# Kernel optimization log

Hardware: AMD Instinct MI355X
Metric: run time of the kernel (lower is better)

Reference implementation:

```python
import jax, jax.numpy as jnp
import numpy as np

N_NODES = 50000
N_EDGES = 1000000
IN_DIM, HID_DIM, OUT_DIM = 128, 64, 16


def setup_inputs() -> dict:
    key = jax.random.key(0)
    k1, k2, k3, k4 = jax.random.split(key, 4)
    x = jax.random.normal(k1, (N_NODES, IN_DIM), dtype=jnp.float32)
    edge_index = jax.random.randint(k2, (2, N_EDGES), 0, N_NODES, dtype=jnp.int64)
    # Glorot-style scaling for weights, zero bias (PyG GCNConv default init style)
    W1 = jax.random.normal(k3, (IN_DIM, HID_DIM), dtype=jnp.float32) * (1.0 / np.sqrt(IN_DIM))
    b1 = jnp.zeros((HID_DIM,), dtype=jnp.float32)
    W2 = jax.random.normal(k4, (HID_DIM, OUT_DIM), dtype=jnp.float32) * (1.0 / np.sqrt(HID_DIM))
    b2 = jnp.zeros((OUT_DIM,), dtype=jnp.float32)
    return {"x": x, "edge_index": edge_index, "W1": W1, "b1": b1, "W2": W2, "b2": b2}


def gcn_conv(x, src, dst, W, b, num_nodes):
    """PyG GCNConv: add self loops, symmetric deg^{-1/2} normalization,
    linear transform, gather-scale-scatter aggregation, bias."""
    # degree includes self loops (src/dst already augmented by caller)
    deg = jax.ops.segment_sum(jnp.ones_like(dst, dtype=x.dtype), dst, num_segments=num_nodes)
    dinv = jnp.where(deg > 0, deg ** -0.5, 0.0)
    norm = dinv[src] * dinv[dst]            # [E']
    h = x @ W                                # [N, F_out] transform before aggregation
    msg = h[src] * norm[:, None]             # gather + scale
    out = jax.ops.segment_sum(msg, dst, num_segments=num_nodes)  # scatter-add
    return out + b


def reference(x, edge_index, W1, b1, W2, b2):
    n = x.shape[0]
    loops = jnp.arange(n, dtype=edge_index.dtype)
    src = jnp.concatenate([edge_index[0], loops])
    dst = jnp.concatenate([edge_index[1], loops])
    h = gcn_conv(x, src, dst, W1, b1, n)
    h = jax.nn.relu(h)
    out = gcn_conv(h, src, dst, W2, b2, n)
    return out
```

## Files before the change

kernel.cpp:

```cpp
#include <hip/hip_runtime.h>
#include <hip/hip_bf16.h>

#define IN_DIM 128
#define HID_DIM 64
#define OUT_DIM 16

#define SSHIFT 7
#define SMASK 127
#define CHUNK 16384
#define CBLK 1024

static __device__ __forceinline__ unsigned short f2bf(float f) {
    unsigned u = __float_as_uint(f);
    unsigned r = u + 0x7fffu + ((u >> 16) & 1u);
    return (unsigned short)(r >> 16);
}
static __device__ __forceinline__ unsigned packbf2(float a, float b) {
    return (unsigned)f2bf(a) | ((unsigned)f2bf(b) << 16);
}
static __device__ __forceinline__ float bflo(unsigned v) { return __uint_as_float(v << 16); }
static __device__ __forceinline__ float bfhi(unsigned v) { return __uint_as_float(v & 0xffff0000u); }

__global__ __launch_bounds__(CBLK) void passA(const int* __restrict__ dst,
                                              int* __restrict__ cm,
                                              int E, int NS, int NSP) {
    __shared__ int cnt[512];
    int t = threadIdx.x;
    for (int s = t; s < NS; s += CBLK) cnt[s] = 0;
    __syncthreads();
    int base = blockIdx.x * CHUNK;
    #pragma unroll 4
    for (int k = 0; k < CHUNK; k += CBLK) {
        int i = base + k + t;
        if (i < E) atomicAdd(&cnt[dst[i] >> SSHIFT], 1);
    }
    __syncthreads();
    for (int s = t; s < NS; s += CBLK) cm[blockIdx.x * NSP + s] = cnt[s];
}

__global__ __launch_bounds__(64) void passB1(int* __restrict__ cm, int* __restrict__ tot,
                                             int B, int NSP) {
    __shared__ int sv[64];
    int t = threadIdx.x, s = blockIdx.x;
    int v = (t < B) ? cm[t * NSP + s] : 0;
    sv[t] = v;
    __syncthreads();
    for (int off = 1; off < 64; off <<= 1) {
        int tmp = (t >= off) ? sv[t - off] : 0;
        __syncthreads();
        sv[t] += tmp;
        __syncthreads();
    }
    if (t < B) cm[t * NSP + s] = sv[t] - v;
    if (t == 63) tot[s] = sv[63];
}

__global__ __launch_bounds__(512) void passB2(const int* __restrict__ tot,
                                              int* __restrict__ sbase, int NS) {
    __shared__ int sv[512];
    int t = threadIdx.x;
    int v = (t < NS) ? tot[t] : 0;
    sv[t] = v;
    __syncthreads();
    for (int off = 1; off < 512; off <<= 1) {
        int tmp = (t >= off) ? sv[t - off] : 0;
        __syncthreads();
        sv[t] += tmp;
        __syncthreads();
    }
    if (t < NS) sbase[t] = sv[t] - v;
}

__global__ __launch_bounds__(CBLK) void passC(const int* __restrict__ src,
                                              const int* __restrict__ dst,
                                              const int* __restrict__ cm,
                                              const int* __restrict__ sbase,
                                              int* __restrict__ eb,
                                              int E, int NS, int NSP) {
    __shared__ int cur[512];
    int t = threadIdx.x, b = blockIdx.x;
    for (int s = t; s < NS; s += CBLK) cur[s] = sbase[s] + cm[b * NSP + s];
    __syncthreads();
    int base = b * CHUNK;
    #pragma unroll 4
    for (int k = 0; k < CHUNK; k += CBLK) {
        int i = base + k + t;
        if (i < E) {
            int d = dst[i];
            int s = d >> SSHIFT;
            int pos = atomicAdd(&cur[s], 1);
            eb[pos] = src[i] | ((d & SMASK) << 17);
        }
    }
}

__global__ __launch_bounds__(256) void passD(const int* __restrict__ eb,
                                             const int* __restrict__ sbase,
                                             const int* __restrict__ tot,
                                             int* __restrict__ csr_src,
                                             int* __restrict__ row_ptr,
                                             float* __restrict__ dinv,
                                             int N, int E, int NS) {
    __shared__ int deg[128], incl[128], cur[128];
    int s = blockIdx.x, t = threadIdx.x;
    if (t < 128) deg[t] = 0;
    __syncthreads();
    int b0 = sbase[s], cnt = tot[s];
    for (int k = t; k < cnt; k += 256) atomicAdd(&deg[eb[b0 + k] >> 17], 1);
    __syncthreads();
    if (t < 128) incl[t] = deg[t];
    __syncthreads();
    for (int off = 1; off < 128; off <<= 1) {
        int tmp = 0;
        if (t < 128 && t >= off) tmp = incl[t - off];
        __syncthreads();
        if (t < 128) incl[t] += tmp;
        __syncthreads();
    }
    if (t < 128) {
        int loff = incl[t] - deg[t];
        cur[t] = b0 + loff;
        int n = (s << SSHIFT) + t;
        if (n < N) {
            row_ptr[n] = b0 + loff;
            dinv[n] = rsqrtf((float)(deg[t] + 1));
        }
    }
    if (s == NS - 1 && t == 0) row_ptr[N] = E;
    __syncthreads();
    for (int k = t; k < cnt; k += 256) {
        int v = eb[b0 + k];
        int dl = v >> 17;
        int p = atomicAdd(&cur[dl], 1);
        csr_src[p] = v & 0x1FFFF;
    }
}

__global__ __launch_bounds__(256) void gemm1_kernel(const float* __restrict__ x,
                                                    const float* __restrict__ W1,
                                                    const float* __restrict__ dinv,
                                                    unsigned* __restrict__ h1u, int N) {
    __shared__ __align__(16) float sW[IN_DIM * HID_DIM];
    __shared__ __align__(16) float sx[16 * IN_DIM];
    int t = threadIdx.x;
    int node0 = blockIdx.x * 16;

    const float4* W4  = (const float4*)W1;
    float4*       sW4 = (float4*)sW;
    for (int i = t; i < (IN_DIM * HID_DIM) / 4; i += 256) sW4[i] = W4[i];

    const float4* x4  = (const float4*)x;
    float4*       sx4 = (float4*)sx;
    for (int i = t; i < (16 * IN_DIM) / 4; i += 256) {
        int r = i >> 5, c = i & 31;
        int n = node0 + r; if (n >= N) n = 0;
        sx4[(r << 5) + c] = x4[(size_t)n * 32 + c];
    }
    __syncthreads();

    int ln = t >> 4, jj = t & 15;
    int n = node0 + ln;
    float4 acc = {0.f, 0.f, 0.f, 0.f};
    const float* xr = sx + ln * IN_DIM;
    #pragma unroll 4
    for (int k = 0; k < IN_DIM; ++k) {
        float  xk = xr[k];
        float4 wv = ((const float4*)(sW + k * HID_DIM))[jj];
        acc.x += xk * wv.x; acc.y += xk * wv.y; acc.z += xk * wv.z; acc.w += xk * wv.w;
    }
    if (n <= N) {
        float dn = (n < N) ? dinv[n] : 0.f;
        uint2 pv;
        pv.x = packbf2(acc.x * dn, acc.y * dn);
        pv.y = packbf2(acc.z * dn, acc.w * dn);
        ((uint2*)(h1u + (size_t)n * 32))[jj] = pv;
    }
}

__global__ __launch_bounds__(256) void agg1_kernel(const unsigned* __restrict__ h1u,
                                                   const int* __restrict__ row_ptr,
                                                   const int* __restrict__ csr_src,
                                                   const float* __restrict__ dinv,
                                                   const float* __restrict__ b1,
                                                   unsigned* __restrict__ h1au, int N) {
    int t = threadIdx.x;
    int n = blockIdx.x * 4 + (t >> 6);
    if (n >= N) return;
    int lane = t & 63;
    int es = lane >> 3;
    int dg = lane & 7;

    int e0 = row_ptr[n], e1 = row_ptr[n + 1];
    const uint4* rb = (const uint4*)h1u;

    float a0 = 0.f, a1 = 0.f, a2 = 0.f, a3 = 0.f,
          a4 = 0.f, a5 = 0.f, a6 = 0.f, a7 = 0.f;

    for (int base = e0 - 1; base < e1; base += 64) {
        int idx = base + lane;
        int sld = N;
        if (idx == e0 - 1) sld = n;
        else if (idx < e1) sld = csr_src[idx];
        int lim = e1 - base;
        int nr = (lim + 7) >> 3;
        nr = (nr + 1) & ~1;
        for (int r = 0; r < nr; r += 2) {
            int sA = __shfl(sld, (r << 3) + es);
            int sB = __shfl(sld, ((r + 1) << 3) + es);
            uint4 vA = rb[(size_t)sA * 8 + dg];
            uint4 vB = rb[(size_t)sB * 8 + dg];
            a0 += bflo(vA.x) + bflo(vB.x);
            a1 += bfhi(vA.x) + bfhi(vB.x);
            a2 += bflo(vA.y) + bflo(vB.y);
            a3 += bfhi(vA.y) + bfhi(vB.y);
            a4 += bflo(vA.z) + bflo(vB.z);
            a5 += bfhi(vA.z) + bfhi(vB.z);
            a6 += bflo(vA.w) + bflo(vB.w);
            a7 += bfhi(vA.w) + bfhi(vB.w);
        }
    }
    #pragma unroll
    for (int m = 8; m <= 32; m <<= 1) {
        a0 += __shfl_xor(a0, m); a1 += __shfl_xor(a1, m);
        a2 += __shfl_xor(a2, m); a3 += __shfl_xor(a3, m);
        a4 += __shfl_xor(a4, m); a5 += __shfl_xor(a5, m);
        a6 += __shfl_xor(a6, m); a7 += __shfl_xor(a7, m);
    }
    if (es == 0) {
        float dn = dinv[n];
        float4 bA = ((const float4*)b1)[2 * dg];
        float4 bB = ((const float4*)b1)[2 * dg + 1];
        float r0 = fmaxf(fmaf(dn, a0, bA.x), 0.f);
        float r1 = fmaxf(fmaf(dn, a1, bA.y), 0.f);
        float r2 = fmaxf(fmaf(dn, a2, bA.z), 0.f);
        float r3 = fmaxf(fmaf(dn, a3, bA.w), 0.f);
        float r4 = fmaxf(fmaf(dn, a4, bB.x), 0.f);
        float r5 = fmaxf(fmaf(dn, a5, bB.y), 0.f);
        float r6 = fmaxf(fmaf(dn, a6, bB.z), 0.f);
        float r7 = fmaxf(fmaf(dn, a7, bB.w), 0.f);
        uint4 pv;
        pv.x = packbf2(r0, r1); pv.y = packbf2(r2, r3);
        pv.z = packbf2(r4, r5); pv.w = packbf2(r6, r7);
        ((uint4*)h1au)[(size_t)n * 8 + dg] = pv;
    }
}

__global__ __launch_bounds__(256) void gemm2_kernel(const unsigned* __restrict__ h1au,
                                                    const float* __restrict__ W2,
                                                    const float* __restrict__ dinv,
                                                    unsigned* __restrict__ h2u, int N) {
    __shared__ __align__(16) float sW[HID_DIM * OUT_DIM];
    __shared__ __align__(16) float sx[16 * HID_DIM];
    int t = threadIdx.x;
    int node0 = blockIdx.x * 16;

    ((float4*)sW)[t] = ((const float4*)W2)[t];
    for (int i = t; i < 512; i += 256) {
        int r = i >> 5, c = i & 31;
        int n = node0 + r; if (n >= N) n = 0;
        unsigned v = h1au[(size_t)n * 32 + c];
        float2 f; f.x = bflo(v); f.y = bfhi(v);
        *(float2*)(sx + r * HID_DIM + 2 * c) = f;
    }
    __syncthreads();

    int ln = t >> 4, j = t & 15;
    float acc = 0.f;
    const float* xr = sx + ln * HID_DIM;
    #pragma unroll 8
    for (int k = 0; k < HID_DIM; ++k) acc += xr[k] * sW[k * OUT_DIM + j];
    int n = node0 + ln;
    float other = __shfl_xor(acc, 1);
    if (n <= N && (j & 1) == 0) {
        float dn = (n < N) ? dinv[n] : 0.f;
        h2u[(size_t)n * 8 + (j >> 1)] = packbf2(acc * dn, other * dn);
    }
}

__global__ __launch_bounds__(256) void agg2_kernel(const unsigned* __restrict__ h2u,
                                                   const int* __restrict__ row_ptr,
                                                   const int* __restrict__ csr_src,
                                                   const float* __restrict__ dinv,
                                                   const float* __restrict__ b2,
                                                   float* __restrict__ out, int N) {
    int t = threadIdx.x;
    int n = blockIdx.x * 4 + (t >> 6);
    if (n >= N) return;
    int lane = t & 63;
    int es = lane >> 2;
    int dg = lane & 3;

    int e0 = row_ptr[n], e1 = row_ptr[n + 1];
    const uint2* rb = (const uint2*)h2u;

    float a0 = 0.f, a1 = 0.f, a2 = 0.f, a3 = 0.f;

    for (int base = e0 - 1; base < e1; base += 64) {
        int idx = base + lane;
        int sld = N;
        if (idx == e0 - 1) sld = n;
        else if (idx < e1) sld = csr_src[idx];
        int lim = e1 - base;
        int nr = (lim + 15) >> 4;
        nr = (nr + 1) & ~1;
        for (int r = 0; r < nr; r += 2) {
            int sA = __shfl(sld, (r << 4) + es);
            int sB = __shfl(sld, ((r + 1) << 4) + es);
            uint2 vA = rb[(size_t)sA * 4 + dg];
            uint2 vB = rb[(size_t)sB * 4 + dg];
            a0 += bflo(vA.x) + bflo(vB.x);
            a1 += bfhi(vA.x) + bfhi(vB.x);
            a2 += bflo(vA.y) + bflo(vB.y);
            a3 += bfhi(vA.y) + bfhi(vB.y);
        }
    }
    #pragma unroll
    for (int m = 4; m <= 32; m <<= 1) {
        a0 += __shfl_xor(a0, m); a1 += __shfl_xor(a1, m);
        a2 += __shfl_xor(a2, m); a3 += __shfl_xor(a3, m);
    }
    if (es == 0) {
        float dn = dinv[n];
        float4 bb = ((const float4*)b2)[dg];
        float4 r;
        r.x = fmaf(dn, a0, bb.x);
        r.y = fmaf(dn, a1, bb.y);
        r.z = fmaf(dn, a2, bb.z);
        r.w = fmaf(dn, a3, bb.w);
        ((float4*)out)[(size_t)n * 4 + dg] = r;
    }
}

extern "C" void kernel_launch(void* const* d_in, const int* in_sizes, int n_in,
                              void* d_out, int out_size, void* d_ws, size_t ws_size,
                              hipStream_t stream) {
    const float* x  = (const float*)d_in[0];
    const int*   ei = (const int*)d_in[1];
    const float* W1 = (const float*)d_in[2];
    const float* b1 = (const float*)d_in[3];
    const float* W2 = (const float*)d_in[4];
    const float* b2 = (const float*)d_in[5];
    float* out = (float*)d_out;

    const int N = in_sizes[0] / IN_DIM;
    const int E = in_sizes[1] / 2;
    const int* src = ei;
    const int* dst = ei + E;

    const int NS  = (N + SMASK) >> SSHIFT;
    const int NSP = NS + 1;
    const int BC  = (E + CHUNK - 1) / CHUNK;

    char* w = (char*)d_ws;
    auto alloc = [&](size_t bytes) -> void* {
        void* p = (void*)w;
        w += (bytes + 255) & ~(size_t)255;
        return p;
    };
    int*      cm      = (int*)     alloc((size_t)BC * NSP * 4);
    int*      tot     = (int*)     alloc((size_t)NS * 4);
    int*      sbase   = (int*)     alloc((size_t)NS * 4);
    int*      eb      = (int*)     alloc((size_t)E * 4);
    int*      csr_src = (int*)     alloc((size_t)E * 4);
    int*      row_ptr = (int*)     alloc((size_t)(N + 1) * 4);
    float*    dinv    = (float*)   alloc((size_t)N * 4);
    unsigned* h1u     = (unsigned*)alloc((size_t)(N + 1) * 32 * 4);
    unsigned* h1au    = (unsigned*)alloc((size_t)(N + 1) * 32 * 4);
    unsigned* h2u     = (unsigned*)alloc((size_t)(N + 1) * 8 * 4);

    const int GB = (N + 16) / 16;
    const int AB = (N + 3) / 4;

    passA <<<BC, CBLK, 0, stream>>>(dst, cm, E, NS, NSP);
    passB1<<<NS, 64,   0, stream>>>(cm, tot, BC, NSP);
    passB2<<<1,  512,  0, stream>>>(tot, sbase, NS);
    passC <<<BC, CBLK, 0, stream>>>(src, dst, cm, sbase, eb, E, NS, NSP);
    passD <<<NS, 256,  0, stream>>>(eb, sbase, tot, csr_src, row_ptr, dinv, N, E, NS);

    gemm1_kernel<<<GB, 256, 0, stream>>>(x, W1, dinv, h1u, N);
    agg1_kernel<<<AB, 256, 0, stream>>>(h1u, row_ptr, csr_src, dinv, b1, h1au, N);
    gemm2_kernel<<<GB, 256, 0, stream>>>(h1au, W2, dinv, h2u, N);
    agg2_kernel<<<AB, 256, 0, stream>>>(h2u, row_ptr, csr_src, dinv, b2, out, N);
}
```

Baseline: 187.4 us.

## Fuse second-layer GEMM into layer-1 aggregation and shrink counting-sort chunks

Folds the 64x16 W2 transform into agg1_kernel. After the shuffle reduction every lane holds the full 64-wide aggregated row, so each lane applies ReLU and bias, multiplies its 8 features by a slice of W2 held in shared memory, and reduces over 8 lanes to write h2 directly. This removes the h1au intermediate buffer, its write and reread, and one kernel launch. Separately, the counting-sort pass uses smaller chunks and blocks (4096/256 instead of 16384/1024), giving more blocks, with the per-bucket scan widened to 256. The padding row of h2 is zeroed inside passB2 because gemm2, which used to write it, is gone.

```diff
diff --git a/kernel.cpp b/kernel.cpp
--- a/kernel.cpp
+++ b/kernel.cpp
@@ -7,8 +7,8 @@
 
 #define SSHIFT 7
 #define SMASK 127
-#define CHUNK 16384
-#define CBLK 1024
+#define CHUNK 4096
+#define CBLK 256
 
 static __device__ __forceinline__ unsigned short f2bf(float f) {
     unsigned u = __float_as_uint(f);
@@ -38,25 +38,27 @@
     for (int s = t; s < NS; s += CBLK) cm[blockIdx.x * NSP + s] = cnt[s];
 }
 
-__global__ __launch_bounds__(64) void passB1(int* __restrict__ cm, int* __restrict__ tot,
-                                             int B, int NSP) {
-    __shared__ int sv[64];
+__global__ __launch_bounds__(256) void passB1(int* __restrict__ cm, int* __restrict__ tot,
+                                              int B, int NSP) {
+    __shared__ int sv[256];
     int t = threadIdx.x, s = blockIdx.x;
     int v = (t < B) ? cm[t * NSP + s] : 0;
     sv[t] = v;
     __syncthreads();
-    for (int off = 1; off < 64; off <<= 1) {
+    for (int off = 1; off < 256; off <<= 1) {
         int tmp = (t >= off) ? sv[t - off] : 0;
         __syncthreads();
         sv[t] += tmp;
         __syncthreads();
     }
     if (t < B) cm[t * NSP + s] = sv[t] - v;
-    if (t == 63) tot[s] = sv[63];
+    if (t == 255) tot[s] = sv[255];
 }
 
 __global__ __launch_bounds__(512) void passB2(const int* __restrict__ tot,
-                                              int* __restrict__ sbase, int NS) {
+                                              int* __restrict__ sbase,
+                                              unsigned* __restrict__ h2u_dummy,
+                                              int NS) {
     __shared__ int sv[512];
     int t = threadIdx.x;
     int v = (t < NS) ? tot[t] : 0;
@@ -69,6 +71,7 @@
         __syncthreads();
     }
     if (t < NS) sbase[t] = sv[t] - v;
+    if (t >= 504) h2u_dummy[t - 504] = 0u;
 }
 
 __global__ __launch_bounds__(CBLK) void passC(const int* __restrict__ src,
@@ -182,8 +185,13 @@
                                                    const int* __restrict__ csr_src,
                                                    const float* __restrict__ dinv,
                                                    const float* __restrict__ b1,
-                                                   unsigned* __restrict__ h1au, int N) {
-    int t = threadIdx.x;
+                                                   const float* __restrict__ W2,
+                                                   unsigned* __restrict__ h2u, int N) {
+    __shared__ __align__(16) float sW[HID_DIM * OUT_DIM];
+    int t = threadIdx.x;
+    ((float4*)sW)[t] = ((const float4*)W2)[t];
+    __syncthreads();
+
     int n = blockIdx.x * 4 + (t >> 6);
     if (n >= N) return;
     int lane = t & 63;
@@ -226,54 +234,35 @@
         a4 += __shfl_xor(a4, m); a5 += __shfl_xor(a5, m);
         a6 += __shfl_xor(a6, m); a7 += __shfl_xor(a7, m);
     }
-    if (es == 0) {
-        float dn = dinv[n];
-        float4 bA = ((const float4*)b1)[2 * dg];
-        float4 bB = ((const float4*)b1)[2 * dg + 1];
-        float r0 = fmaxf(fmaf(dn, a0, bA.x), 0.f);
-        float r1 = fmaxf(fmaf(dn, a1, bA.y), 0.f);
-        float r2 = fmaxf(fmaf(dn, a2, bA.z), 0.f);
-        float r3 = fmaxf(fmaf(dn, a3, bA.w), 0.f);
-        float r4 = fmaxf(fmaf(dn, a4, bB.x), 0.f);
-        float r5 = fmaxf(fmaf(dn, a5, bB.y), 0.f);
-        float r6 = fmaxf(fmaf(dn, a6, bB.z), 0.f);
-        float r7 = fmaxf(fmaf(dn, a7, bB.w), 0.f);
-        uint4 pv;
-        pv.x = packbf2(r0, r1); pv.y = packbf2(r2, r3);
-        pv.z = packbf2(r4, r5); pv.w = packbf2(r6, r7);
-        ((uint4*)h1au)[(size_t)n * 8 + dg] = pv;
-    }
-}
-
-__global__ __launch_bounds__(256) void gemm2_kernel(const unsigned* __restrict__ h1au,
-                                                    const float* __restrict__ W2,
-                                                    const float* __restrict__ dinv,
-                                                    unsigned* __restrict__ h2u, int N) {
-    __shared__ __align__(16) float sW[HID_DIM * OUT_DIM];
-    __shared__ __align__(16) float sx[16 * HID_DIM];
-    int t = threadIdx.x;
-    int node0 = blockIdx.x * 16;
-
-    ((float4*)sW)[t] = ((const float4*)W2)[t];
-    for (int i = t; i < 512; i += 256) {
-        int r = i >> 5, c = i & 31;
-        int n = node0 + r; if (n >= N) n = 0;
-        unsigned v = h1au[(size_t)n * 32 + c];
-        float2 f; f.x = bflo(v); f.y = bfhi(v);
-        *(float2*)(sx + r * HID_DIM + 2 * c) = f;
-    }
-    __syncthreads();
-
-    int ln = t >> 4, j = t & 15;
-    float acc = 0.f;
-    const float* xr = sx + ln * HID_DIM;
-    #pragma unroll 8
-    for (int k = 0; k < HID_DIM; ++k) acc += xr[k] * sW[k * OUT_DIM + j];
-    int n = node0 + ln;
-    float other = __shfl_xor(acc, 1);
-    if (n <= N && (j & 1) == 0) {
-        float dn = (n < N) ? dinv[n] : 0.f;
-        h2u[(size_t)n * 8 + (j >> 1)] = packbf2(acc * dn, other * dn);
+    float dn = dinv[n];
+    float4 bA = ((const float4*)b1)[2 * dg];
+    float4 bB = ((const float4*)b1)[2 * dg + 1];
+    float r0 = fmaxf(fmaf(dn, a0, bA.x), 0.f);
+    float r1 = fmaxf(fmaf(dn, a1, bA.y), 0.f);
+    float r2 = fmaxf(fmaf(dn, a2, bA.z), 0.f);
+    float r3 = fmaxf(fmaf(dn, a3, bA.w), 0.f);
+    float r4 = fmaxf(fmaf(dn, a4, bB.x), 0.f);
+    float r5 = fmaxf(fmaf(dn, a5, bB.y), 0.f);
+    float r6 = fmaxf(fmaf(dn, a6, bB.z), 0.f);
+    float r7 = fmaxf(fmaf(dn, a7, bB.w), 0.f);
+
+    const float* wrow = sW + (8 * dg) * OUT_DIM + 2 * es;
+    float p0 = 0.f, p1 = 0.f;
+    #pragma unroll
+    for (int i = 0; i < 8; ++i) {
+        float2 wv = *(const float2*)(wrow + i * OUT_DIM);
+        float ri = (i == 0) ? r0 : (i == 1) ? r1 : (i == 2) ? r2 : (i == 3) ? r3
+                 : (i == 4) ? r4 : (i == 5) ? r5 : (i == 6) ? r6 : r7;
+        p0 = fmaf(ri, wv.x, p0);
+        p1 = fmaf(ri, wv.y, p1);
+    }
+    #pragma unroll
+    for (int m = 1; m <= 4; m <<= 1) {
+        p0 += __shfl_xor(p0, m);
+        p1 += __shfl_xor(p1, m);
+    }
+    if (dg == 0) {
+        h2u[(size_t)n * 8 + es] = packbf2(p0 * dn, p1 * dn);
     }
 }
 
@@ -357,7 +346,7 @@
         w += (bytes + 255) & ~(size_t)255;
         return p;
     };
-    int*      cm      = (int*)     alloc((size_t)BC * NSP * 4);
+    int*      cm      = (int*)     alloc((size_t)256 * NSP * 4);
     int*      tot     = (int*)     alloc((size_t)NS * 4);
     int*      sbase   = (int*)     alloc((size_t)NS * 4);
     int*      eb      = (int*)     alloc((size_t)E * 4);
@@ -365,20 +354,18 @@
     int*      row_ptr = (int*)     alloc((size_t)(N + 1) * 4);
     float*    dinv    = (float*)   alloc((size_t)N * 4);
     unsigned* h1u     = (unsigned*)alloc((size_t)(N + 1) * 32 * 4);
-    unsigned* h1au    = (unsigned*)alloc((size_t)(N + 1) * 32 * 4);
     unsigned* h2u     = (unsigned*)alloc((size_t)(N + 1) * 8 * 4);
 
     const int GB = (N + 16) / 16;
     const int AB = (N + 3) / 4;
 
     passA <<<BC, CBLK, 0, stream>>>(dst, cm, E, NS, NSP);
-    passB1<<<NS, 64,   0, stream>>>(cm, tot, BC, NSP);
-    passB2<<<1,  512,  0, stream>>>(tot, sbase, NS);
+    passB1<<<NS, 256,  0, stream>>>(cm, tot, BC, NSP);
+    passB2<<<1,  512,  0, stream>>>(tot, sbase, h2u + (size_t)N * 8, NS);
     passC <<<BC, CBLK, 0, stream>>>(src, dst, cm, sbase, eb, E, NS, NSP);
     passD <<<NS, 256,  0, stream>>>(eb, sbase, tot, csr_src, row_ptr, dinv, N, E, NS);
 
     gemm1_kernel<<<GB, 256, 0, stream>>>(x, W1, dinv, h1u, N);
-    agg1_kernel<<<AB, 256, 0, stream>>>(h1u, row_ptr, csr_src, dinv, b1, h1au, N);
-    gemm2_kernel<<<GB, 256, 0, stream>>>(h1au, W2, dinv, h2u, N);
+    agg1_kernel<<<AB, 256, 0, stream>>>(h1u, row_ptr, csr_src, dinv, b1, W2, h2u, N);
     agg2_kernel<<<AB, 256, 0, stream>>>(h2u, row_ptr, csr_src, dinv, b2, out, N);
 }
```

Measured after the change: 195.0 us. +4.0%, slower.

## Drop the global bucket-scan kernel and shrink histogram chunks for more blocks

Applied to the files above, without the earlier changes.

Removes the single-block passB2 scan launch. Each passC block now recomputes the bucket prefix over per-bucket totals in shared memory, and passD computes its own base offset by reducing the totals of the preceding buckets. Histogram chunks shrink from 16384 to 4096 edges with 256-thread blocks, so passA and passC get more blocks (about 245 instead of 62), and passB1 now scans up to 256 block counts. This trades one serialized kernel launch for redundant per-block scan work. It relies on the block count staying at or below 256, since cm is sized for 256 rows.

```diff
diff --git a/kernel.cpp b/kernel.cpp
--- a/kernel.cpp
+++ b/kernel.cpp
@@ -7,8 +7,8 @@
 
 #define SSHIFT 7
 #define SMASK 127
-#define CHUNK 16384
-#define CBLK 1024
+#define CHUNK 4096
+#define CBLK 256
 
 static __device__ __forceinline__ unsigned short f2bf(float f) {
     unsigned u = __float_as_uint(f);
@@ -38,48 +38,46 @@
     for (int s = t; s < NS; s += CBLK) cm[blockIdx.x * NSP + s] = cnt[s];
 }
 
-__global__ __launch_bounds__(64) void passB1(int* __restrict__ cm, int* __restrict__ tot,
-                                             int B, int NSP) {
-    __shared__ int sv[64];
+__global__ __launch_bounds__(256) void passB1(int* __restrict__ cm, int* __restrict__ tot,
+                                              int B, int NSP) {
+    __shared__ int sv[256];
     int t = threadIdx.x, s = blockIdx.x;
     int v = (t < B) ? cm[t * NSP + s] : 0;
     sv[t] = v;
     __syncthreads();
-    for (int off = 1; off < 64; off <<= 1) {
+    for (int off = 1; off < 256; off <<= 1) {
         int tmp = (t >= off) ? sv[t - off] : 0;
         __syncthreads();
         sv[t] += tmp;
         __syncthreads();
     }
     if (t < B) cm[t * NSP + s] = sv[t] - v;
-    if (t == 63) tot[s] = sv[63];
-}
-
-__global__ __launch_bounds__(512) void passB2(const int* __restrict__ tot,
-                                              int* __restrict__ sbase, int NS) {
-    __shared__ int sv[512];
-    int t = threadIdx.x;
-    int v = (t < NS) ? tot[t] : 0;
-    sv[t] = v;
-    __syncthreads();
-    for (int off = 1; off < 512; off <<= 1) {
-        int tmp = (t >= off) ? sv[t - off] : 0;
-        __syncthreads();
-        sv[t] += tmp;
-        __syncthreads();
-    }
-    if (t < NS) sbase[t] = sv[t] - v;
+    if (t == 255) tot[s] = sv[255];
 }
 
 __global__ __launch_bounds__(CBLK) void passC(const int* __restrict__ src,
                                               const int* __restrict__ dst,
                                               const int* __restrict__ cm,
-                                              const int* __restrict__ sbase,
+                                              const int* __restrict__ tot,
                                               int* __restrict__ eb,
                                               int E, int NS, int NSP) {
+    __shared__ int sb[512];
     __shared__ int cur[512];
     int t = threadIdx.x, b = blockIdx.x;
-    for (int s = t; s < NS; s += CBLK) cur[s] = sbase[s] + cm[b * NSP + s];
+    int i0 = t, i1 = t + 256;
+    int v0 = (i0 < NS) ? tot[i0] : 0;
+    int v1 = (i1 < NS) ? tot[i1] : 0;
+    sb[i0] = v0; sb[i1] = v1;
+    __syncthreads();
+    for (int off = 1; off < 512; off <<= 1) {
+        int t0 = (i0 >= off) ? sb[i0 - off] : 0;
+        int t1 = (i1 >= off) ? sb[i1 - off] : 0;
+        __syncthreads();
+        sb[i0] += t0; sb[i1] += t1;
+        __syncthreads();
+    }
+    if (i0 < NS) cur[i0] = (sb[i0] - v0) + cm[b * NSP + i0];
+    if (i1 < NS) cur[i1] = (sb[i1] - v1) + cm[b * NSP + i1];
     __syncthreads();
     int base = b * CHUNK;
     #pragma unroll 4
@@ -95,17 +93,25 @@
 }
 
 __global__ __launch_bounds__(256) void passD(const int* __restrict__ eb,
-                                             const int* __restrict__ sbase,
                                              const int* __restrict__ tot,
                                              int* __restrict__ csr_src,
                                              int* __restrict__ row_ptr,
                                              float* __restrict__ dinv,
                                              int N, int E, int NS) {
+    __shared__ int red[256];
     __shared__ int deg[128], incl[128], cur[128];
     int s = blockIdx.x, t = threadIdx.x;
     if (t < 128) deg[t] = 0;
-    __syncthreads();
-    int b0 = sbase[s], cnt = tot[s];
+    int part = 0;
+    for (int k = t; k < s; k += 256) part += tot[k];
+    red[t] = part;
+    __syncthreads();
+    for (int off = 128; off >= 1; off >>= 1) {
+        if (t < off) red[t] += red[t + off];
+        __syncthreads();
+    }
+    int b0 = red[0];
+    int cnt = tot[s];
     for (int k = t; k < cnt; k += 256) atomicAdd(&deg[eb[b0 + k] >> 17], 1);
     __syncthreads();
     if (t < 128) incl[t] = deg[t];
@@ -357,9 +363,8 @@
         w += (bytes + 255) & ~(size_t)255;
         return p;
     };
-    int*      cm      = (int*)     alloc((size_t)BC * NSP * 4);
+    int*      cm      = (int*)     alloc((size_t)256 * NSP * 4);
     int*      tot     = (int*)     alloc((size_t)NS * 4);
-    int*      sbase   = (int*)     alloc((size_t)NS * 4);
     int*      eb      = (int*)     alloc((size_t)E * 4);
     int*      csr_src = (int*)     alloc((size_t)E * 4);
     int*      row_ptr = (int*)     alloc((size_t)(N + 1) * 4);
@@ -372,10 +377,9 @@
     const int AB = (N + 3) / 4;
 
     passA <<<BC, CBLK, 0, stream>>>(dst, cm, E, NS, NSP);
-    passB1<<<NS, 64,   0, stream>>>(cm, tot, BC, NSP);
-    passB2<<<1,  512,  0, stream>>>(tot, sbase, NS);
-    passC <<<BC, CBLK, 0, stream>>>(src, dst, cm, sbase, eb, E, NS, NSP);
-    passD <<<NS, 256,  0, stream>>>(eb, sbase, tot, csr_src, row_ptr, dinv, N, E, NS);
+    passB1<<<NS, 256,  0, stream>>>(cm, tot, BC, NSP);
+    passC <<<BC, CBLK, 0, stream>>>(src, dst, cm, tot, eb, E, NS, NSP);
+    passD <<<NS, 256,  0, stream>>>(eb, tot, csr_src, row_ptr, dinv, N, E, NS);
 
     gemm1_kernel<<<GB, 256, 0, stream>>>(x, W1, dinv, h1u, N);
     agg1_kernel<<<AB, 256, 0, stream>>>(h1u, row_ptr, csr_src, dinv, b1, h1au, N);
```

New measurement: 186.3 us. Within noise of the previous version (-0.6%).
